# Performance work log

Hardware: AMD Instinct MI355X
Metric: run time of the kernel (lower is better)

## Reference

```python
import jax, jax.numpy as jnp
import numpy as np

EPS = 1e-5
N_HEADS = 8


def _ln(x, g, b):
    m = jnp.mean(x, -1, keepdims=True)
    v = jnp.mean((x - m) ** 2, -1, keepdims=True)
    return (x - m) * jax.lax.rsqrt(v + EPS) * g + b


def setup_inputs() -> dict:
    key = jax.random.key(0)
    ks = jax.random.split(key, 24)
    B, T, H = 64, 512, 256
    HH, H2 = H // 2, 2 * H
    w = lambda k, shape, fan_in: jax.random.normal(k, shape, jnp.float32) / np.sqrt(fan_in)
    return {
        "state": jax.random.normal(ks[0], (B, T, H), jnp.float32),
        "action": jax.random.normal(ks[1], (B, T, 2), jnp.float32),
        "ae_w1": w(ks[2], (2, HH), 2), "ae_b1": jnp.zeros((HH,), jnp.float32),
        "ae_w2": w(ks[3], (HH, H), HH), "ae_b2": jnp.zeros((H,), jnp.float32),
        "ln1_g": jnp.ones((H,), jnp.float32), "ln1_b": jnp.zeros((H,), jnp.float32),
        "ln2_g": jnp.ones((H,), jnp.float32), "ln2_b": jnp.zeros((H,), jnp.float32),
        "wq": w(ks[4], (H, H), H), "bq": jnp.zeros((H,), jnp.float32),
        "wk": w(ks[5], (H, H), H), "bk": jnp.zeros((H,), jnp.float32),
        "wv": w(ks[6], (H, H), H), "bv": jnp.zeros((H,), jnp.float32),
        "wo": w(ks[7], (H, H), H), "bo": jnp.zeros((H,), jnp.float32),
        "gru_wih": w(ks[8], (H, 3 * H2), H), "gru_bih": jnp.zeros((3 * H2,), jnp.float32),
        "gru_whh": w(ks[9], (H2, 3 * H2), H2), "gru_bhh": jnp.zeros((3 * H2,), jnp.float32),
        "mlp_w": w(ks[10], (H2, H), H2), "mlp_b": jnp.zeros((H,), jnp.float32),
    }


def reference(state, action, ae_w1, ae_b1, ae_w2, ae_b2, ln1_g, ln1_b, ln2_g, ln2_b,
              wq, bq, wk, bk, wv, bv, wo, bo,
              gru_wih, gru_bih, gru_whh, gru_bhh, mlp_w, mlp_b):
    B, T, H = state.shape
    dH = H // N_HEADS
    # action encoder (vectorized over all timesteps at once)
    ae = jax.nn.relu(action @ ae_w1 + ae_b1) @ ae_w2 + ae_b2  # [B,T,H]
    q_in = _ln(state, ln1_g, ln1_b)
    kv_in = _ln(ae, ln2_g, ln2_b)
    qh = (q_in @ wq + bq).reshape(B, T, N_HEADS, dH)
    kh = (kv_in @ wk + bk).reshape(B, T, N_HEADS, dH)
    vh = (kv_in @ wv + bv).reshape(B, T, N_HEADS, dH)
    # single query / single key per (b,t): softmax over the length-1 key axis == 1
    scores = jnp.sum(qh * kh, -1, keepdims=True) / jnp.sqrt(jnp.asarray(dH, state.dtype))
    attn = jax.nn.softmax(scores, axis=-1)  # [B,T,nH,1] of ones
    attended = (attn * vh).reshape(B, T, H) @ wo + bo
    x = state + attended  # [B,T,H]
    # GRU: original uses batch_first=False on a [B,T,H] tensor, so the
    # recurrence runs over dim 0 (B) with T as the effective batch.
    H2 = gru_whh.shape[0]

    def step(h, x_t):  # h,[T,2H]; x_t [T,H]
        gi = x_t @ gru_wih + gru_bih
        gh = h @ gru_whh + gru_bhh
        i_r, i_z, i_n = jnp.split(gi, 3, -1)
        h_r, h_z, h_n = jnp.split(gh, 3, -1)
        r = jax.nn.sigmoid(i_r + h_r)
        z = jax.nn.sigmoid(i_z + h_z)
        n = jnp.tanh(i_n + r * h_n)
        h_new = (1.0 - z) * n + z * h
        return h_new, h_new

    h0 = jnp.zeros((T, H2), x.dtype)
    _, out = jax.lax.scan(step, h0, x)  # [B,T,2H]
    states = out @ mlp_w + mlp_b  # dropout is identity in eval mode
    return states, states[:, -1]
```

## Files before the change

### kernel.cpp

```cpp
#include <hip/hip_runtime.h>
#include <hip/hip_bf16.h>

typedef unsigned short u16;
typedef unsigned long long u64;
typedef __attribute__((ext_vector_type(8))) short bf16x8;
typedef __attribute__((ext_vector_type(4))) float f32x4;

static __device__ __forceinline__ u16 f2bf(float f) {
    union { float f; unsigned u; } cv; cv.f = f;
    unsigned u = cv.u;
    unsigned r = u + 0x7FFF + ((u >> 16) & 1);
    return (u16)(r >> 16);
}
static __device__ __forceinline__ float bf2f(u16 b) {
    union { unsigned u; float f; } cv; cv.u = ((unsigned)b) << 16;
    return cv.f;
}
static __device__ __forceinline__ float sigmoidf_(float x) {
    return 1.0f / (1.0f + __expf(-x));
}
static __device__ __forceinline__ float tanhf_(float x) {
    float e = __expf(-2.f * fabsf(x));
    float t = (1.f - e) / (1.f + e);
    return copysignf(t, x);
}

__global__ __launch_bounds__(256) void prep_all(
    const float* __restrict__ wv, const float* __restrict__ wo,
    const float* __restrict__ wih, const float* __restrict__ whh,
    const float* __restrict__ mlp, const float* __restrict__ w2,
    const float* __restrict__ bv, const float* __restrict__ bo,
    u16* __restrict__ wv_bf, u16* __restrict__ woT, u16* __restrict__ wihT,
    u16* __restrict__ whhT, u16* __restrict__ mlpT, u16* __restrict__ w2T,
    float* __restrict__ bfv, float* __restrict__ zerob,
    u16* __restrict__ h0_bf, unsigned* __restrict__ flags)
{
    __shared__ u16 t[64][66];
    int bid = blockIdx.x, tid = threadIdx.x;

    if (bid < 64) {
        int i = (bid * 256 + tid) * 4;
        float4 v = *(const float4*)&wv[i];
        u16 pack[4] = { f2bf(v.x), f2bf(v.y), f2bf(v.z), f2bf(v.w) };
        *(u64*)&wv_bf[i] = *(u64*)pack;
        return;
    }
    if (bid == 408) {
        int j = tid;
        float s = bo[j];
        for (int k = 0; k < 256; ++k) s = fmaf(bv[k], wo[k * 256 + j], s);
        bfv[j] = s;
        zerob[j] = 0.f;
        return;
    }
    if (bid >= 409 && bid < 537) {
        int i = ((bid - 409) * 256 + tid) * 2;
        u64* p = (u64*)h0_bf;
        p[i] = 0; p[i + 1] = 0;
        return;
    }
    if (bid == 537) {
        unsigned* p = flags;
        for (int i = tid; i < 32 * 8 * 32; i += 256) p[i] = 0u;
        return;
    }

    const float* src; u16* dst; int K, N, bx, by;
    if (bid < 80)       { src = wo;  dst = woT;  K = 256; N = 256;  int l = bid - 64;  bx = l & 3; by = l >> 2; }
    else if (bid < 176) { src = wih; dst = wihT; K = 256; N = 1536; int l = bid - 80;  bx = l & 3; by = l >> 2; }
    else if (bid < 368) { src = whh; dst = whhT; K = 512; N = 1536; int l = bid - 176; bx = l & 7; by = l >> 3; }
    else if (bid < 400) { src = mlp; dst = mlpT; K = 512; N = 256;  int l = bid - 368; bx = l & 7; by = l >> 3; }
    else                { src = w2;  dst = w2T;  K = 128; N = 256;  int l = bid - 400; bx = l & 1; by = l >> 1; }

    int k0 = bx * 64, n0 = by * 64;
    int r = tid >> 4, c4 = (tid & 15) * 4;
#pragma unroll
    for (int p = 0; p < 4; ++p) {
        int row = r + p * 16;
        float4 v = *(const float4*)&src[(size_t)(k0 + row) * N + n0 + c4];
        t[c4 + 0][row] = f2bf(v.x);
        t[c4 + 1][row] = f2bf(v.y);
        t[c4 + 2][row] = f2bf(v.z);
        t[c4 + 3][row] = f2bf(v.w);
    }
    __syncthreads();
    int rr = tid >> 3, cc = (tid & 7) * 8;
#pragma unroll
    for (int p = 0; p < 2; ++p) {
        int row = rr + p * 32;
        u16 pack[8];
#pragma unroll
        for (int j = 0; j < 8; ++j) pack[j] = t[row][cc + j];
        *(uint4*)&dst[(size_t)(n0 + row) * K + k0 + cc] = *(uint4*)pack;
    }
}

__global__ __launch_bounds__(256) void ae_ln_mfma(
    const float* __restrict__ action,
    const float* __restrict__ w1, const float* __restrict__ b1,
    const u16* __restrict__ w2T, const float* __restrict__ b2,
    const float* __restrict__ g, const float* __restrict__ be,
    u16* __restrict__ kvbf)
{
    __shared__ u16 lB[256][136];
    __shared__ u16 lA[64][136];
    int tid = threadIdx.x;
    long base = (long)blockIdx.x * 64;

    for (int idx = tid; idx < 256 * 16; idx += 256) {
        int r = idx >> 4, ch = (idx & 15) * 8;
        *(uint4*)&lB[r][ch] = *(const uint4*)&w2T[r * 128 + ch];
    }
    for (int idx = tid; idx < 8192; idx += 256) {
        int r = idx >> 7, k = idx & 127;
        float a0 = action[(base + r) * 2], a1 = action[(base + r) * 2 + 1];
        float v = fmaf(a1, w1[128 + k], fmaf(a0, w1[k], b1[k]));
        lA[r][k] = f2bf(v > 0.f ? v : 0.f);
    }
    __syncthreads();

    int wv = tid >> 6, l = tid & 63;
    int fr = l & 15, fq = l >> 4;
    f32x4 acc[4][4] = {};
#pragma unroll
    for (int ks = 0; ks < 4; ++ks) {
        bf16x8 a[4], b[4];
#pragma unroll
        for (int mi = 0; mi < 4; ++mi) a[mi] = *(bf16x8*)&lA[mi * 16 + fr][ks * 32 + fq * 8];
#pragma unroll
        for (int ni = 0; ni < 4; ++ni) b[ni] = *(bf16x8*)&lB[wv * 64 + ni * 16 + fr][ks * 32 + fq * 8];
#pragma unroll
        for (int mi = 0; mi < 4; ++mi)
#pragma unroll
            for (int ni = 0; ni < 4; ++ni)
                acc[mi][ni] = __builtin_amdgcn_mfma_f32_16x16x32_bf16(a[mi], b[ni], acc[mi][ni], 0, 0, 0);
    }
    __syncthreads();

    float* e = (float*)&lB[0][0];
#pragma unroll
    for (int mi = 0; mi < 4; ++mi)
#pragma unroll
        for (int ni = 0; ni < 4; ++ni) {
            int col = wv * 64 + ni * 16 + fr;
            float bb = b2[col];
#pragma unroll
            for (int reg = 0; reg < 4; ++reg)
                e[(mi * 16 + fq * 4 + reg) * 261 + col] = acc[mi][ni][reg] + bb;
        }
    __syncthreads();

    int t = tid >> 2, sub = tid & 3;
    float s = 0.f, ss = 0.f;
#pragma unroll
    for (int i = 0; i < 64; ++i) {
        float v = e[t * 261 + sub + i * 4];
        s += v; ss += v * v;
    }
    s += __shfl_xor(s, 1); ss += __shfl_xor(ss, 1);
    s += __shfl_xor(s, 2); ss += __shfl_xor(ss, 2);
    float m = s * (1.f / 256.f);
    float var = ss * (1.f / 256.f) - m * m;
    float rs = rsqrtf(var + 1e-5f);
#pragma unroll
    for (int i8 = 0; i8 < 8; ++i8) {
        u16 pack[8];
#pragma unroll
        for (int j = 0; j < 8; ++j) {
            int col = sub * 64 + i8 * 8 + j;
            float v = (e[t * 261 + col] - m) * rs * g[col] + be[col];
            pack[j] = f2bf(v);
        }
        *(uint4*)&kvbf[(base + t) * 256 + sub * 64 + i8 * 8] = *(uint4*)pack;
    }
}

template <int MODE>
__global__ __launch_bounds__(256) void gemm128(
    const u16* __restrict__ A, const u16* __restrict__ BT,
    const float* __restrict__ bias, const float* __restrict__ resid,
    u16* __restrict__ outBf, float* __restrict__ outF,
    int N, int K)
{
    __shared__ u16 lA[128][72];
    __shared__ u16 lB[128][72];
    int tid = threadIdx.x;
    int bm = blockIdx.x * 128, bn = blockIdx.y * 128;

    f32x4 acc[4][4] = {};
    int w = tid >> 6, l = tid & 63;
    int wr = (w >> 1) * 64, wc = (w & 1) * 64;
    int fr = l & 15, fk = (l >> 4) * 8;

    for (int k0 = 0; k0 < K; k0 += 64) {
#pragma unroll
        for (int i = 0; i < 4; ++i) {
            int idx = tid + i * 256;
            int r = idx >> 3, c8 = (idx & 7) * 8;
            *(uint4*)&lA[r][c8] = *(const uint4*)&A[(long)(bm + r) * K + k0 + c8];
            *(uint4*)&lB[r][c8] = *(const uint4*)&BT[(long)(bn + r) * K + k0 + c8];
        }
        __syncthreads();
#pragma unroll
        for (int half = 0; half < 2; ++half) {
            int fo = half * 32 + fk;
            bf16x8 a[4], b[4];
#pragma unroll
            for (int mi = 0; mi < 4; ++mi) a[mi] = *(bf16x8*)&lA[wr + mi * 16 + fr][fo];
#pragma unroll
            for (int ni = 0; ni < 4; ++ni) b[ni] = *(bf16x8*)&lB[wc + ni * 16 + fr][fo];
#pragma unroll
            for (int mi = 0; mi < 4; ++mi)
#pragma unroll
                for (int ni = 0; ni < 4; ++ni)
                    acc[mi][ni] = __builtin_amdgcn_mfma_f32_16x16x32_bf16(a[mi], b[ni], acc[mi][ni], 0, 0, 0);
        }
        __syncthreads();
    }

#pragma unroll
    for (int mi = 0; mi < 4; ++mi)
#pragma unroll
        for (int ni = 0; ni < 4; ++ni) {
            int c = bn + wc + ni * 16 + fr;
            float bz = bias[c];
#pragma unroll
            for (int reg = 0; reg < 4; ++reg) {
                int r = bm + wr + mi * 16 + (l >> 4) * 4 + reg;
                float v = acc[mi][ni][reg] + bz;
                if constexpr (MODE == 0) {
                    v += resid[(long)r * N + c];
                    outBf[(long)r * N + c] = f2bf(v);
                } else if constexpr (MODE == 1) {
                    outBf[(long)r * N + c] = f2bf(v);
                } else {
                    outF[(long)r * N + c] = v;
                    if ((r & 511) == 511) outF[8388608 + (long)(r >> 9) * N + c] = v;
                }
            }
        }
}

__global__ __launch_bounds__(768, 1) void gru_persistent6(
    const u16* __restrict__ whhT, const float* __restrict__ bhh,
    const u16* __restrict__ gi_bf, const u16* __restrict__ h0_bf,
    u16* __restrict__ out_bf, unsigned* __restrict__ flags)
{
    __shared__ u64 lh64[2048];
    __shared__ __align__(16) float ghs[3][16][68];
    u16* lh = (u16*)lh64;

    int tid = threadIdx.x;
    int bid = blockIdx.x;
    int tg = bid >> 3, cb = bid & 7;
    int tbase = tg * 16, cbase = cb * 64;

    int w = tid >> 6, l = tid & 63;
    int fr = l & 15, fo = l >> 4;
    int cpos = w & 3, gate = w >> 2;

    bf16x8 a[16];
    {
        const u16* wp = whhT + ((size_t)(gate << 9) + cbase + cpos * 16 + fr) * 512 + fo * 8;
#pragma unroll
        for (int kk = 0; kk < 16; ++kk)
            a[kk] = *(const bf16x8*)(wp + kk * 32);
    }

    int et = tid >> 5, ec = (tid & 31) * 2;
    bool ep = tid < 512;
    float hreg0 = 0.f, hreg1 = 0.f;
    float bh_r0 = 0, bh_r1 = 0, bh_z0 = 0, bh_z1 = 0, bh_n0 = 0, bh_n1 = 0;
    if (ep) {
        bh_r0 = bhh[cbase + ec];        bh_r1 = bhh[cbase + ec + 1];
        bh_z0 = bhh[512 + cbase + ec];  bh_z1 = bhh[512 + cbase + ec + 1];
        bh_n0 = bhh[1024 + cbase + ec]; bh_n1 = bhh[1024 + cbase + ec + 1];
    }

    const unsigned* gp = (const unsigned*)gi_bf;
    unsigned g_r = 0, g_z = 0, g_n = 0;
    if (ep) {
        size_t grow = (size_t)(tbase + et) * 1536;
        g_r = gp[(grow + cbase + ec) >> 1];
        g_z = gp[(grow + 512 + cbase + ec) >> 1];
        g_n = gp[(grow + 1024 + cbase + ec) >> 1];
    }

    for (int step = 0; step < 64; ++step) {
        const u64* hb64 = (const u64*)(step ? out_bf + (size_t)(step - 1) * 262144
                                           : h0_bf);
#pragma unroll
        for (int i = 0; i < 3; ++i) {
            int idx = tid + i * 768;
            if (idx < 2048) {
                int r = idx >> 7, kw = idx & 127;
                u64 v = __hip_atomic_load(hb64 + (size_t)(tbase + r) * 128 + kw,
                                          __ATOMIC_RELAXED, __HIP_MEMORY_SCOPE_AGENT);
                lh64[r * 128 + (kw ^ ((r & 7) << 1))] = v;
            }
        }
        __syncthreads();

        f32x4 acc = {0.f, 0.f, 0.f, 0.f};
#pragma unroll
        for (int kk = 0; kk < 16; ++kk) {
            int kb = kk * 32 + fo * 8;
            bf16x8 b = *(bf16x8*)&lh[fr * 512 + (kb ^ ((fr & 7) << 3))];
            acc = __builtin_amdgcn_mfma_f32_16x16x32_bf16(a[kk], b, acc, 0, 0, 0);
        }
        *(f32x4*)&ghs[gate][fr][cpos * 16 + fo * 4] = acc;
        __syncthreads();

        if (ep) {
            float ghr0 = ghs[0][et][ec], ghr1 = ghs[0][et][ec + 1];
            float ghz0 = ghs[1][et][ec], ghz1 = ghs[1][et][ec + 1];
            float ghn0 = ghs[2][et][ec], ghn1 = ghs[2][et][ec + 1];
            float r0 = sigmoidf_(bf2f((u16)(g_r & 0xffff)) + ghr0 + bh_r0);
            float r1 = sigmoidf_(bf2f((u16)(g_r >> 16)) + ghr1 + bh_r1);
            float z0 = sigmoidf_(bf2f((u16)(g_z & 0xffff)) + ghz0 + bh_z0);
            float z1 = sigmoidf_(bf2f((u16)(g_z >> 16)) + ghz1 + bh_z1);
            float n0 = tanhf_(bf2f((u16)(g_n & 0xffff)) + r0 * (ghn0 + bh_n0));
            float n1 = tanhf_(bf2f((u16)(g_n >> 16)) + r1 * (ghn1 + bh_n1));
            hreg0 = (1.f - z0) * n0 + z0 * hreg0;
            hreg1 = (1.f - z1) * n1 + z1 * hreg1;
            unsigned packv = (unsigned)f2bf(hreg0) | ((unsigned)f2bf(hreg1) << 16);
            __hip_atomic_store(
                (unsigned*)out_bf + ((((size_t)step * 512 + tbase + et) * 512 + cbase + ec) >> 1),
                packv, __ATOMIC_RELAXED, __HIP_MEMORY_SCOPE_AGENT);
        }
        __syncthreads();

        if (step < 63) {
            if (tid == 0)
                __hip_atomic_store(&flags[(tg * 8 + cb) * 32], (unsigned)(step + 1),
                                   __ATOMIC_RELAXED, __HIP_MEMORY_SCOPE_AGENT);
            if (ep) {
                size_t grow = ((size_t)(step + 1) * 512 + tbase + et) * 1536;
                g_r = gp[(grow + cbase + ec) >> 1];
                g_z = gp[(grow + 512 + cbase + ec) >> 1];
                g_n = gp[(grow + 1024 + cbase + ec) >> 1];
            }
            if (tid < 8) {
                unsigned tgt = (unsigned)(step + 1);
                while (__hip_atomic_load(&flags[(tg * 8 + tid) * 32],
                                         __ATOMIC_RELAXED, __HIP_MEMORY_SCOPE_AGENT) < tgt)
                    __builtin_amdgcn_s_sleep(1);
            }
            __syncthreads();
        }
    }
}

extern "C" void kernel_launch(void* const* d_in, const int* in_sizes, int n_in,
                              void* d_out, int out_size, void* d_ws, size_t ws_size,
                              hipStream_t stream)
{
    const float* state   = (const float*)d_in[0];
    const float* action  = (const float*)d_in[1];
    const float* ae_w1   = (const float*)d_in[2];
    const float* ae_b1   = (const float*)d_in[3];
    const float* ae_w2   = (const float*)d_in[4];
    const float* ae_b2   = (const float*)d_in[5];
    const float* ln2_g   = (const float*)d_in[8];
    const float* ln2_b   = (const float*)d_in[9];
    const float* wv      = (const float*)d_in[14];
    const float* bv      = (const float*)d_in[15];
    const float* wo      = (const float*)d_in[16];
    const float* bo      = (const float*)d_in[17];
    const float* gru_wih = (const float*)d_in[18];
    const float* gru_bih = (const float*)d_in[19];
    const float* gru_whh = (const float*)d_in[20];
    const float* gru_bhh = (const float*)d_in[21];
    const float* mlp_w   = (const float*)d_in[22];
    const float* mlp_b   = (const float*)d_in[23];

    char* ws = (char*)d_ws;
    size_t off = 0;
    auto carve = [&](size_t bytes) -> char* {
        char* p = ws + off; off = (off + bytes + 255) & ~(size_t)255; return p;
    };
    u16*   kv_bf  = (u16*)carve(32768ull * 256 * 2);
    u16*   x_bf   = (u16*)carve(32768ull * 256 * 2);
    u16*   gi_bf  = (u16*)carve(32768ull * 1536 * 2);
    u16*   out_bf = (u16*)carve(32768ull * 512 * 2);
    u16*   WfT    = (u16*)carve(256 * 256 * 2);
    float* bfv    = (float*)carve(256 * 4);
    u16*   wihT   = (u16*)carve(1536 * 256 * 2);
    u16*   whhT   = (u16*)carve(1536 * 512 * 2);
    u16*   mlpT   = (u16*)carve(256 * 512 * 2);
    u16*   w2T    = (u16*)carve(256 * 128 * 2);
    u16*   woT    = (u16*)carve(256 * 256 * 2);
    u16*   wv_bf  = (u16*)carve(256 * 256 * 2);
    float* zerob  = (float*)carve(256 * 4);
    u16*   h0_bf  = (u16*)carve(512 * 512 * 2);
    unsigned* flags = (unsigned*)carve(32 * 8 * 32 * 4);

    prep_all<<<538, 256, 0, stream>>>(wv, wo, gru_wih, gru_whh, mlp_w, ae_w2,
                                      bv, bo, wv_bf, woT, wihT, whhT, mlpT, w2T,
                                      bfv, zerob, h0_bf, flags);

    gemm128<1><<<dim3(2, 2), 256, 0, stream>>>(woT, wv_bf, zerob, nullptr, WfT, nullptr, 256, 256);

    ae_ln_mfma<<<512, 256, 0, stream>>>(action, ae_w1, ae_b1, w2T, ae_b2,
                                        ln2_g, ln2_b, kv_bf);

    gemm128<0><<<dim3(256, 2), 256, 0, stream>>>(kv_bf, WfT, bfv, state, x_bf, nullptr, 256, 256);
    gemm128<1><<<dim3(256, 12), 256, 0, stream>>>(x_bf, wihT, gru_bih, nullptr, gi_bf, nullptr, 1536, 256);

    {
        void* args[] = { (void*)&whhT, (void*)&gru_bhh, (void*)&gi_bf,
                         (void*)&h0_bf, (void*)&out_bf, (void*)&flags };
        hipError_t cerr = hipLaunchCooperativeKernel((const void*)gru_persistent6,
                                                     dim3(256), dim3(768), args, 0, stream);
        if (cerr != hipSuccess) {
            gru_persistent6<<<dim3(256), dim3(768), 0, stream>>>(
                whhT, gru_bhh, gi_bf, h0_bf, out_bf, flags);
        }
    }

    gemm128<2><<<dim3(256, 2), 256, 0, stream>>>(out_bf, mlpT, mlp_b, nullptr, nullptr,
                                                 (float*)d_out, 256, 512);
}
```

Baseline: 359.7 us.

## Fuse output MLP projection into persistent GRU kernel using idle waves

The final MLP GEMM over all GRU outputs is folded into the persistent GRU kernel. Waves 8-9, which sit idle during the gate epilogue, project the previous step's hidden state (already staged in shared memory) through mlp_w, and an extra iteration handles the last step. The flag wait moves to the top of the loop. This removes one kernel launch and a separate re-read of the hidden-state sequence, at the cost of extra registers and MFMA work per step inside the latency-critical recurrence.

```diff
diff --git a/kernel.cpp b/kernel.cpp
--- a/kernel.cpp
+++ b/kernel.cpp
@@ -231,20 +231,19 @@
                 if constexpr (MODE == 0) {
                     v += resid[(long)r * N + c];
                     outBf[(long)r * N + c] = f2bf(v);
-                } else if constexpr (MODE == 1) {
+                } else {
                     outBf[(long)r * N + c] = f2bf(v);
-                } else {
-                    outF[(long)r * N + c] = v;
-                    if ((r & 511) == 511) outF[8388608 + (long)(r >> 9) * N + c] = v;
                 }
             }
         }
 }
 
-__global__ __launch_bounds__(768, 1) void gru_persistent6(
+__global__ __launch_bounds__(768, 1) void gru_persistent9(
     const u16* __restrict__ whhT, const float* __restrict__ bhh,
     const u16* __restrict__ gi_bf, const u16* __restrict__ h0_bf,
-    u16* __restrict__ out_bf, unsigned* __restrict__ flags)
+    const u16* __restrict__ mlpT, const float* __restrict__ mlp_b,
+    u16* __restrict__ out_bf, float* __restrict__ dout,
+    unsigned* __restrict__ flags)
 {
     __shared__ u64 lh64[2048];
     __shared__ __align__(16) float ghs[3][16][68];
@@ -265,6 +264,18 @@
 #pragma unroll
         for (int kk = 0; kk < 16; ++kk)
             a[kk] = *(const bf16x8*)(wp + kk * 32);
+    }
+
+    int mtile = w - 8;
+    bool mw = (mtile >= 0 && mtile < 2);
+    bf16x8 am[16];
+    f32x4 bm = {0.f, 0.f, 0.f, 0.f};
+    if (mw) {
+        const u16* mp = mlpT + ((size_t)(cb * 32 + mtile * 16 + fr)) * 512 + fo * 8;
+#pragma unroll
+        for (int kk = 0; kk < 16; ++kk)
+            am[kk] = *(const bf16x8*)(mp + kk * 32);
+        bm = *(const f32x4*)&mlp_b[cb * 32 + mtile * 16 + fo * 4];
     }
 
     int et = tid >> 5, ec = (tid & 31) * 2;
@@ -286,9 +297,18 @@
         g_n = gp[(grow + 1024 + cbase + ec) >> 1];
     }
 
-    for (int step = 0; step < 64; ++step) {
-        const u64* hb64 = (const u64*)(step ? out_bf + (size_t)(step - 1) * 262144
-                                           : h0_bf);
+    for (int s = 0; s <= 64; ++s) {
+        if (s >= 1) {
+            if (tid < 8) {
+                unsigned tgt = (unsigned)s;
+                while (__hip_atomic_load(&flags[(tg * 8 + tid) * 32],
+                                         __ATOMIC_RELAXED, __HIP_MEMORY_SCOPE_AGENT) < tgt)
+                    __builtin_amdgcn_s_sleep(1);
+            }
+            __syncthreads();
+        }
+        const u64* hb64 = (const u64*)(s ? out_bf + (size_t)(s - 1) * 262144
+                                         : h0_bf);
 #pragma unroll
         for (int i = 0; i < 3; ++i) {
             int idx = tid + i * 768;
@@ -301,52 +321,75 @@
         }
         __syncthreads();
 
-        f32x4 acc = {0.f, 0.f, 0.f, 0.f};
-#pragma unroll
-        for (int kk = 0; kk < 16; ++kk) {
-            int kb = kk * 32 + fo * 8;
-            bf16x8 b = *(bf16x8*)&lh[fr * 512 + (kb ^ ((fr & 7) << 3))];
-            acc = __builtin_amdgcn_mfma_f32_16x16x32_bf16(a[kk], b, acc, 0, 0, 0);
-        }
-        *(f32x4*)&ghs[gate][fr][cpos * 16 + fo * 4] = acc;
-        __syncthreads();
-
-        if (ep) {
-            float ghr0 = ghs[0][et][ec], ghr1 = ghs[0][et][ec + 1];
-            float ghz0 = ghs[1][et][ec], ghz1 = ghs[1][et][ec + 1];
-            float ghn0 = ghs[2][et][ec], ghn1 = ghs[2][et][ec + 1];
-            float r0 = sigmoidf_(bf2f((u16)(g_r & 0xffff)) + ghr0 + bh_r0);
-            float r1 = sigmoidf_(bf2f((u16)(g_r >> 16)) + ghr1 + bh_r1);
-            float z0 = sigmoidf_(bf2f((u16)(g_z & 0xffff)) + ghz0 + bh_z0);
-            float z1 = sigmoidf_(bf2f((u16)(g_z >> 16)) + ghz1 + bh_z1);
-            float n0 = tanhf_(bf2f((u16)(g_n & 0xffff)) + r0 * (ghn0 + bh_n0));
-            float n1 = tanhf_(bf2f((u16)(g_n >> 16)) + r1 * (ghn1 + bh_n1));
-            hreg0 = (1.f - z0) * n0 + z0 * hreg0;
-            hreg1 = (1.f - z1) * n1 + z1 * hreg1;
-            unsigned packv = (unsigned)f2bf(hreg0) | ((unsigned)f2bf(hreg1) << 16);
-            __hip_atomic_store(
-                (unsigned*)out_bf + ((((size_t)step * 512 + tbase + et) * 512 + cbase + ec) >> 1),
-                packv, __ATOMIC_RELAXED, __HIP_MEMORY_SCOPE_AGENT);
-        }
-        __syncthreads();
-
-        if (step < 63) {
+        if (s < 64) {
+            f32x4 acc = {0.f, 0.f, 0.f, 0.f};
+#pragma unroll
+            for (int kk = 0; kk < 16; ++kk) {
+                int kb = kk * 32 + fo * 8;
+                bf16x8 b = *(bf16x8*)&lh[fr * 512 + (kb ^ ((fr & 7) << 3))];
+                acc = __builtin_amdgcn_mfma_f32_16x16x32_bf16(a[kk], b, acc, 0, 0, 0);
+            }
+            *(f32x4*)&ghs[gate][fr][cpos * 16 + fo * 4] = acc;
+            __syncthreads();
+
+            if (ep) {
+                float ghr0 = ghs[0][et][ec], ghr1 = ghs[0][et][ec + 1];
+                float ghz0 = ghs[1][et][ec], ghz1 = ghs[1][et][ec + 1];
+                float ghn0 = ghs[2][et][ec], ghn1 = ghs[2][et][ec + 1];
+                float r0 = sigmoidf_(bf2f((u16)(g_r & 0xffff)) + ghr0 + bh_r0);
+                float r1 = sigmoidf_(bf2f((u16)(g_r >> 16)) + ghr1 + bh_r1);
+                float z0 = sigmoidf_(bf2f((u16)(g_z & 0xffff)) + ghz0 + bh_z0);
+                float z1 = sigmoidf_(bf2f((u16)(g_z >> 16)) + ghz1 + bh_z1);
+                float n0 = tanhf_(bf2f((u16)(g_n & 0xffff)) + r0 * (ghn0 + bh_n0));
+                float n1 = tanhf_(bf2f((u16)(g_n >> 16)) + r1 * (ghn1 + bh_n1));
+                hreg0 = (1.f - z0) * n0 + z0 * hreg0;
+                hreg1 = (1.f - z1) * n1 + z1 * hreg1;
+                unsigned packv = (unsigned)f2bf(hreg0) | ((unsigned)f2bf(hreg1) << 16);
+                __hip_atomic_store(
+                    (unsigned*)out_bf + ((((size_t)s * 512 + tbase + et) * 512 + cbase + ec) >> 1),
+                    packv, __ATOMIC_RELAXED, __HIP_MEMORY_SCOPE_AGENT);
+            } else if (mw && s >= 1) {
+                f32x4 accm = {0.f, 0.f, 0.f, 0.f};
+#pragma unroll
+                for (int kk = 0; kk < 16; ++kk) {
+                    int kb = kk * 32 + fo * 8;
+                    bf16x8 b = *(bf16x8*)&lh[fr * 512 + (kb ^ ((fr & 7) << 3))];
+                    accm = __builtin_amdgcn_mfma_f32_16x16x32_bf16(am[kk], b, accm, 0, 0, 0);
+                }
+                accm += bm;
+                size_t rowt = (size_t)(s - 1) * 512 + tbase + fr;
+                int colb = cb * 32 + mtile * 16 + fo * 4;
+                *(f32x4*)&dout[rowt * 256 + colb] = accm;
+                if (tg == 31 && fr == 15)
+                    *(f32x4*)&dout[8388608 + (size_t)(s - 1) * 256 + colb] = accm;
+            }
+            __syncthreads();
+
             if (tid == 0)
-                __hip_atomic_store(&flags[(tg * 8 + cb) * 32], (unsigned)(step + 1),
+                __hip_atomic_store(&flags[(tg * 8 + cb) * 32], (unsigned)(s + 1),
                                    __ATOMIC_RELAXED, __HIP_MEMORY_SCOPE_AGENT);
-            if (ep) {
-                size_t grow = ((size_t)(step + 1) * 512 + tbase + et) * 1536;
+            if (ep && s < 63) {
+                size_t grow = ((size_t)(s + 1) * 512 + tbase + et) * 1536;
                 g_r = gp[(grow + cbase + ec) >> 1];
                 g_z = gp[(grow + 512 + cbase + ec) >> 1];
                 g_n = gp[(grow + 1024 + cbase + ec) >> 1];
             }
-            if (tid < 8) {
-                unsigned tgt = (unsigned)(step + 1);
-                while (__hip_atomic_load(&flags[(tg * 8 + tid) * 32],
-                                         __ATOMIC_RELAXED, __HIP_MEMORY_SCOPE_AGENT) < tgt)
-                    __builtin_amdgcn_s_sleep(1);
-            }
-            __syncthreads();
+        } else {
+            if (mw) {
+                f32x4 accm = {0.f, 0.f, 0.f, 0.f};
+#pragma unroll
+                for (int kk = 0; kk < 16; ++kk) {
+                    int kb = kk * 32 + fo * 8;
+                    bf16x8 b = *(bf16x8*)&lh[fr * 512 + (kb ^ ((fr & 7) << 3))];
+                    accm = __builtin_amdgcn_mfma_f32_16x16x32_bf16(am[kk], b, accm, 0, 0, 0);
+                }
+                accm += bm;
+                size_t rowt = (size_t)63 * 512 + tbase + fr;
+                int colb = cb * 32 + mtile * 16 + fo * 4;
+                *(f32x4*)&dout[rowt * 256 + colb] = accm;
+                if (tg == 31 && fr == 15)
+                    *(f32x4*)&dout[8388608 + (size_t)63 * 256 + colb] = accm;
+            }
         }
     }
 }
@@ -408,16 +451,15 @@
     gemm128<1><<<dim3(256, 12), 256, 0, stream>>>(x_bf, wihT, gru_bih, nullptr, gi_bf, nullptr, 1536, 256);
 
     {
+        float* doutf = (float*)d_out;
         void* args[] = { (void*)&whhT, (void*)&gru_bhh, (void*)&gi_bf,
-                         (void*)&h0_bf, (void*)&out_bf, (void*)&flags };
-        hipError_t cerr = hipLaunchCooperativeKernel((const void*)gru_persistent6,
+                         (void*)&h0_bf, (void*)&mlpT, (void*)&mlp_b,
+                         (void*)&out_bf, (void*)&doutf, (void*)&flags };
+        hipError_t cerr = hipLaunchCooperativeKernel((const void*)gru_persistent9,
                                                      dim3(256), dim3(768), args, 0, stream);
         if (cerr != hipSuccess) {
-            gru_persistent6<<<dim3(256), dim3(768), 0, stream>>>(
-                whhT, gru_bhh, gi_bf, h0_bf, out_bf, flags);
-        }
-    }
-
-    gemm128<2><<<dim3(256, 2), 256, 0, stream>>>(out_bf, mlpT, mlp_b, nullptr, nullptr,
-                                                 (float*)d_out, 256, 512);
-}
+            gru_persistent9<<<dim3(256), dim3(768), 0, stream>>>(
+                whhT, gru_bhh, gi_bf, h0_bf, mlpT, mlp_b, out_bf, (float*)d_out, flags);
+        }
+    }
+}
```

New measurement: 421.3 us. +17.1%, slower.

## Halve GRU persistent grid by giving each block 128 hidden columns

Applied to the files above, without the earlier changes.

The persistent GRU kernel now runs 128 blocks instead of 256. Each block holds two halves of the recurrent weight slice in registers and computes 128 columns per step with two MFMA accumulators. The epilogue handles four columns per thread with 64-bit gi loads and h stores, and each block waits on 4 peer flags instead of 8. This cuts inter-block synchronization fan-in and hidden-state reloads per column. The cost is doubled per-block MFMA work, higher register pressure, and fewer CUs in use.

```diff
diff --git a/kernel.cpp b/kernel.cpp
--- a/kernel.cpp
+++ b/kernel.cpp
@@ -241,49 +241,54 @@
         }
 }
 
-__global__ __launch_bounds__(768, 1) void gru_persistent6(
+__global__ __launch_bounds__(768, 1) void gru_persistent10(
     const u16* __restrict__ whhT, const float* __restrict__ bhh,
     const u16* __restrict__ gi_bf, const u16* __restrict__ h0_bf,
     u16* __restrict__ out_bf, unsigned* __restrict__ flags)
 {
     __shared__ u64 lh64[2048];
-    __shared__ __align__(16) float ghs[3][16][68];
+    __shared__ __align__(16) float ghs[3][16][132];
     u16* lh = (u16*)lh64;
 
     int tid = threadIdx.x;
     int bid = blockIdx.x;
-    int tg = bid >> 3, cb = bid & 7;
-    int tbase = tg * 16, cbase = cb * 64;
+    int tg = bid >> 2, cb = bid & 3;
+    int tbase = tg * 16, cbase = cb * 128;
 
     int w = tid >> 6, l = tid & 63;
     int fr = l & 15, fo = l >> 4;
-    int cpos = w & 3, gate = w >> 2;
-
-    bf16x8 a[16];
-    {
-        const u16* wp = whhT + ((size_t)(gate << 9) + cbase + cpos * 16 + fr) * 512 + fo * 8;
+    int cp = w & 3, gate = w >> 2;
+
+    bf16x8 a[2][16];
+#pragma unroll
+    for (int half = 0; half < 2; ++half) {
+        const u16* wp = whhT + ((size_t)(gate << 9) + cbase + half * 64 + cp * 16 + fr) * 512 + fo * 8;
 #pragma unroll
         for (int kk = 0; kk < 16; ++kk)
-            a[kk] = *(const bf16x8*)(wp + kk * 32);
-    }
-
-    int et = tid >> 5, ec = (tid & 31) * 2;
+            a[half][kk] = *(const bf16x8*)(wp + kk * 32);
+    }
+
+    int et = tid >> 5, ec = (tid & 31) * 4;
     bool ep = tid < 512;
-    float hreg0 = 0.f, hreg1 = 0.f;
-    float bh_r0 = 0, bh_r1 = 0, bh_z0 = 0, bh_z1 = 0, bh_n0 = 0, bh_n1 = 0;
+    float hreg[4] = {0.f, 0.f, 0.f, 0.f};
+    float bh_r[4], bh_z[4], bh_n[4];
+#pragma unroll
+    for (int j = 0; j < 4; ++j) { bh_r[j] = bh_z[j] = bh_n[j] = 0.f; }
     if (ep) {
-        bh_r0 = bhh[cbase + ec];        bh_r1 = bhh[cbase + ec + 1];
-        bh_z0 = bhh[512 + cbase + ec];  bh_z1 = bhh[512 + cbase + ec + 1];
-        bh_n0 = bhh[1024 + cbase + ec]; bh_n1 = bhh[1024 + cbase + ec + 1];
-    }
-
-    const unsigned* gp = (const unsigned*)gi_bf;
-    unsigned g_r = 0, g_z = 0, g_n = 0;
+#pragma unroll
+        for (int j = 0; j < 4; ++j) {
+            bh_r[j] = bhh[cbase + ec + j];
+            bh_z[j] = bhh[512 + cbase + ec + j];
+            bh_n[j] = bhh[1024 + cbase + ec + j];
+        }
+    }
+
+    u64 g_r = 0, g_z = 0, g_n = 0;
     if (ep) {
         size_t grow = (size_t)(tbase + et) * 1536;
-        g_r = gp[(grow + cbase + ec) >> 1];
-        g_z = gp[(grow + 512 + cbase + ec) >> 1];
-        g_n = gp[(grow + 1024 + cbase + ec) >> 1];
+        g_r = *(const u64*)&gi_bf[grow + cbase + ec];
+        g_z = *(const u64*)&gi_bf[grow + 512 + cbase + ec];
+        g_n = *(const u64*)&gi_bf[grow + 1024 + cbase + ec];
     }
 
     for (int step = 0; step < 64; ++step) {
@@ -301,48 +306,48 @@
         }
         __syncthreads();
 
-        f32x4 acc = {0.f, 0.f, 0.f, 0.f};
+        f32x4 acc0 = {0.f, 0.f, 0.f, 0.f}, acc1 = acc0;
 #pragma unroll
         for (int kk = 0; kk < 16; ++kk) {
             int kb = kk * 32 + fo * 8;
             bf16x8 b = *(bf16x8*)&lh[fr * 512 + (kb ^ ((fr & 7) << 3))];
-            acc = __builtin_amdgcn_mfma_f32_16x16x32_bf16(a[kk], b, acc, 0, 0, 0);
-        }
-        *(f32x4*)&ghs[gate][fr][cpos * 16 + fo * 4] = acc;
+            acc0 = __builtin_amdgcn_mfma_f32_16x16x32_bf16(a[0][kk], b, acc0, 0, 0, 0);
+            acc1 = __builtin_amdgcn_mfma_f32_16x16x32_bf16(a[1][kk], b, acc1, 0, 0, 0);
+        }
+        *(f32x4*)&ghs[gate][fr][cp * 16 + fo * 4] = acc0;
+        *(f32x4*)&ghs[gate][fr][64 + cp * 16 + fo * 4] = acc1;
         __syncthreads();
 
         if (ep) {
-            float ghr0 = ghs[0][et][ec], ghr1 = ghs[0][et][ec + 1];
-            float ghz0 = ghs[1][et][ec], ghz1 = ghs[1][et][ec + 1];
-            float ghn0 = ghs[2][et][ec], ghn1 = ghs[2][et][ec + 1];
-            float r0 = sigmoidf_(bf2f((u16)(g_r & 0xffff)) + ghr0 + bh_r0);
-            float r1 = sigmoidf_(bf2f((u16)(g_r >> 16)) + ghr1 + bh_r1);
-            float z0 = sigmoidf_(bf2f((u16)(g_z & 0xffff)) + ghz0 + bh_z0);
-            float z1 = sigmoidf_(bf2f((u16)(g_z >> 16)) + ghz1 + bh_z1);
-            float n0 = tanhf_(bf2f((u16)(g_n & 0xffff)) + r0 * (ghn0 + bh_n0));
-            float n1 = tanhf_(bf2f((u16)(g_n >> 16)) + r1 * (ghn1 + bh_n1));
-            hreg0 = (1.f - z0) * n0 + z0 * hreg0;
-            hreg1 = (1.f - z1) * n1 + z1 * hreg1;
-            unsigned packv = (unsigned)f2bf(hreg0) | ((unsigned)f2bf(hreg1) << 16);
+            u16 pack[4];
+#pragma unroll
+            for (int j = 0; j < 4; ++j) {
+                float rg = sigmoidf_(bf2f((u16)(g_r >> (16 * j))) + ghs[0][et][ec + j] + bh_r[j]);
+                float zg = sigmoidf_(bf2f((u16)(g_z >> (16 * j))) + ghs[1][et][ec + j] + bh_z[j]);
+                float ng = tanhf_(bf2f((u16)(g_n >> (16 * j))) + rg * (ghs[2][et][ec + j] + bh_n[j]));
+                hreg[j] = (1.f - zg) * ng + zg * hreg[j];
+                pack[j] = f2bf(hreg[j]);
+            }
+            u64 pk = *(u64*)pack;
             __hip_atomic_store(
-                (unsigned*)out_bf + ((((size_t)step * 512 + tbase + et) * 512 + cbase + ec) >> 1),
-                packv, __ATOMIC_RELAXED, __HIP_MEMORY_SCOPE_AGENT);
+                (u64*)out_bf + ((((size_t)step * 512 + tbase + et) * 512 + cbase + ec) >> 2),
+                pk, __ATOMIC_RELAXED, __HIP_MEMORY_SCOPE_AGENT);
         }
         __syncthreads();
 
         if (step < 63) {
             if (tid == 0)
-                __hip_atomic_store(&flags[(tg * 8 + cb) * 32], (unsigned)(step + 1),
+                __hip_atomic_store(&flags[(tg * 4 + cb) * 32], (unsigned)(step + 1),
                                    __ATOMIC_RELAXED, __HIP_MEMORY_SCOPE_AGENT);
             if (ep) {
                 size_t grow = ((size_t)(step + 1) * 512 + tbase + et) * 1536;
-                g_r = gp[(grow + cbase + ec) >> 1];
-                g_z = gp[(grow + 512 + cbase + ec) >> 1];
-                g_n = gp[(grow + 1024 + cbase + ec) >> 1];
+                g_r = *(const u64*)&gi_bf[grow + cbase + ec];
+                g_z = *(const u64*)&gi_bf[grow + 512 + cbase + ec];
+                g_n = *(const u64*)&gi_bf[grow + 1024 + cbase + ec];
             }
-            if (tid < 8) {
+            if (tid < 4) {
                 unsigned tgt = (unsigned)(step + 1);
-                while (__hip_atomic_load(&flags[(tg * 8 + tid) * 32],
+                while (__hip_atomic_load(&flags[(tg * 4 + tid) * 32],
                                          __ATOMIC_RELAXED, __HIP_MEMORY_SCOPE_AGENT) < tgt)
                     __builtin_amdgcn_s_sleep(1);
             }
@@ -410,10 +415,10 @@
     {
         void* args[] = { (void*)&whhT, (void*)&gru_bhh, (void*)&gi_bf,
                          (void*)&h0_bf, (void*)&out_bf, (void*)&flags };
-        hipError_t cerr = hipLaunchCooperativeKernel((const void*)gru_persistent6,
-                                                     dim3(256), dim3(768), args, 0, stream);
+        hipError_t cerr = hipLaunchCooperativeKernel((const void*)gru_persistent10,
+                                                     dim3(128), dim3(768), args, 0, stream);
         if (cerr != hipSuccess) {
-            gru_persistent6<<<dim3(256), dim3(768), 0, stream>>>(
+            gru_persistent10<<<dim3(128), dim3(768), 0, stream>>>(
                 whhT, gru_bhh, gi_bf, h0_bf, out_bf, flags);
         }
     }
```

Measured after the change: 569.4 us. 58.3% more time.
